# Kernel optimization log

Hardware: AMD Instinct MI355X
Metric: run time of the kernel (lower is better)

The kernel has to match this reference:

```python
import jax, jax.numpy as jnp
import numpy as np

G, K, N, T = 16, 2048, 2048, 16384  # groups, in_features, out_features, total_tokens


def setup_inputs() -> dict:
    key = jax.random.key(0)
    k1, k2 = jax.random.split(key)
    hidden_states = jax.random.normal(k1, (T, K), dtype=jnp.float32)
    # kaiming_uniform_(a=sqrt(5)) on [G, K, N] -> bound = sqrt(6 / ((1 + 5) * fan_in)) = 1/sqrt(K)
    bound = 1.0 / np.sqrt(K)
    weight = jax.random.uniform(k2, (G, K, N), dtype=jnp.float32, minval=-bound, maxval=bound)
    tokens_per_group = T // G
    tokens_per_expert = jnp.full((G,), tokens_per_group, dtype=jnp.int32)
    # offsets[0] = 0, offsets[i] = start of group i (matches _group_sizes_from_offsets)
    offsets = jnp.arange(G, dtype=jnp.int32) * tokens_per_group
    blockscale_offsets = offsets  # unused by the eager math path; carried for signature fidelity
    return {
        "hidden_states": hidden_states,
        "weight": weight,
        "offsets": offsets,
        "blockscale_offsets": blockscale_offsets,
        "tokens_per_expert": tokens_per_expert,
    }


def reference(hidden_states, weight, offsets, blockscale_offsets, tokens_per_expert):
    # Grouped (ragged) GEMM: rows [offsets[g] : offsets[g]+tokens_per_expert[g]] of
    # hidden_states are multiplied by weight[g] ([K, N]). tokens_per_expert equals the
    # group sizes derived from offsets in the torch module's eager fallback.
    # jax.lax.ragged_dot is the exact grouped-mm primitive (no dense [T,K,N] gather).
    return jax.lax.ragged_dot(hidden_states, weight, tokens_per_expert)
```

## Files before the change

### kernel.cpp

```cpp
#include <hip/hip_runtime.h>
#include <cstdint>
#include <cstddef>

#define GRP 16
#define KD  2048
#define ND  2048
#define TD  16384

#define BM 128
#define BN 128
#define BK 64
#define NT (KD / BK)

typedef __bf16 bf16x8 __attribute__((ext_vector_type(8)));
typedef float  f32x4  __attribute__((ext_vector_type(4)));

__device__ __forceinline__ uint32_t pk2bf(float x, float y) {
  uint32_t ux = __builtin_bit_cast(uint32_t, x);
  uint32_t uy = __builtin_bit_cast(uint32_t, y);
  ux += 0x7fffu + ((ux >> 16) & 1u);
  uy += 0x7fffu + ((uy >> 16) & 1u);
  return __builtin_amdgcn_perm(uy, ux, 0x07060302);
}

__device__ __forceinline__ int find_group(const int* tokens, int row0) {
  int g = GRP - 1, start = 0;
  for (int i = 0; i < GRP; ++i) {
    int sz = tokens[i];
    if (row0 < start + sz) { g = i; break; }
    start += sz;
  }
  return g;
}

__global__ __launch_bounds__(256, 2)
void fused_gemm(const float* __restrict__ A, const float* __restrict__ W,
                const int* __restrict__ tokens, float* __restrict__ C) {
  __shared__ uint16_t Alds[BM * BK];
  __shared__ uint16_t Blds[BN * BK];

  const int t    = threadIdx.x;
  const int n0   = blockIdx.x * BN;
  const int row0 = blockIdx.y * BM;

  const int g = find_group(tokens, row0);
  const float* Wg = W + (size_t)g * KD * ND;

  const int lane = t & 63;
  const int wid  = t >> 6;
  const int wm   = wid & 1;
  const int wn   = wid >> 1;
  const int l16  = lane & 15;
  const int quad = lane >> 4;

  const float* aptr[4];
  uint32_t*    adst[4];
  for (int i = 0; i < 4; ++i) {
    const int c  = t + 256 * i;
    const int r  = c >> 3;
    const int cl = c & 7;
    aptr[i] = A + (size_t)(row0 + r) * KD + cl * 8;
    adst[i] = (uint32_t*)&Alds[(r * 8 + (cl ^ (r & 7))) * 8];
  }

  const int nl = t & 127;
  const int bh = t >> 7;
  const float* bptr = Wg + (size_t)(bh * 32) * ND + n0 + nl;
  uint32_t* bdst[4];
  for (int c = 0; c < 4; ++c) {
    const int kc = bh * 4 + c;
    bdst[c] = (uint32_t*)&Blds[(nl * 8 + (kc ^ (nl & 7))) * 8];
  }

  int aoff[2][4], boff[2][4];
  for (int h = 0; h < 2; ++h) {
    for (int mi = 0; mi < 4; ++mi) {
      const int r = wm * 64 + mi * 16 + l16;
      aoff[h][mi] = r * BK + (((h * 4 + quad) ^ (r & 7)) * 8);
    }
    for (int ni = 0; ni < 4; ++ni) {
      const int r = wn * 64 + ni * 16 + l16;
      boff[h][ni] = r * BK + (((h * 4 + quad) ^ (r & 7)) * 8);
    }
  }

  f32x4 acc[4][4] = {};

  float4 ar[4][2];
  float  br[4][8];

  auto issue = [&](int k0) {
    #pragma unroll
    for (int i = 0; i < 4; ++i) {
      ar[i][0] = *(const float4*)(aptr[i] + k0);
      ar[i][1] = *(const float4*)(aptr[i] + k0 + 4);
    }
    const float* bp = bptr + (size_t)k0 * ND;
    #pragma unroll
    for (int c = 0; c < 4; ++c)
      #pragma unroll
      for (int j = 0; j < 8; ++j)
        br[c][j] = bp[(size_t)(c * 8 + j) * ND];
  };

  issue(0);

  for (int kt = 0; kt < NT; ++kt) {
    __syncthreads();

    #pragma unroll
    for (int i = 0; i < 4; ++i) {
      uint4 p;
      p.x = pk2bf(ar[i][0].x, ar[i][0].y);
      p.y = pk2bf(ar[i][0].z, ar[i][0].w);
      p.z = pk2bf(ar[i][1].x, ar[i][1].y);
      p.w = pk2bf(ar[i][1].z, ar[i][1].w);
      *(uint4*)adst[i] = p;
    }
    #pragma unroll
    for (int c = 0; c < 4; ++c) {
      uint4 p;
      p.x = pk2bf(br[c][0], br[c][1]);
      p.y = pk2bf(br[c][2], br[c][3]);
      p.z = pk2bf(br[c][4], br[c][5]);
      p.w = pk2bf(br[c][6], br[c][7]);
      *(uint4*)bdst[c] = p;
    }

    if (kt + 1 < NT) issue((kt + 1) * BK);

    __syncthreads();

    #pragma unroll
    for (int h = 0; h < 2; ++h) {
      bf16x8 af[4], bfr[4];
      #pragma unroll
      for (int mi = 0; mi < 4; ++mi) af[mi]  = *(const bf16x8*)&Alds[aoff[h][mi]];
      #pragma unroll
      for (int ni = 0; ni < 4; ++ni) bfr[ni] = *(const bf16x8*)&Blds[boff[h][ni]];
      #pragma unroll
      for (int mi = 0; mi < 4; ++mi)
        #pragma unroll
        for (int ni = 0; ni < 4; ++ni)
          acc[mi][ni] = __builtin_amdgcn_mfma_f32_16x16x32_bf16(af[mi], bfr[ni],
                                                                acc[mi][ni], 0, 0, 0);
    }
  }

  #pragma unroll
  for (int mi = 0; mi < 4; ++mi) {
    const int m = row0 + wm * 64 + mi * 16 + quad * 4;
    #pragma unroll
    for (int ni = 0; ni < 4; ++ni) {
      const int n = n0 + wn * 64 + ni * 16 + l16;
      #pragma unroll
      for (int r = 0; r < 4; ++r)
        C[(size_t)(m + r) * ND + n] = acc[mi][ni][r];
    }
  }
}

extern "C" void kernel_launch(void* const* d_in, const int* in_sizes, int n_in,
                              void* d_out, int out_size, void* d_ws, size_t ws_size,
                              hipStream_t stream) {
  const float* hidden = (const float*)d_in[0];
  const float* weight = (const float*)d_in[1];
  const int*   tokens = (const int*)d_in[4];
  float* out = (float*)d_out;
  (void)d_ws; (void)ws_size;

  fused_gemm<<<dim3(ND / BN, TD / BM), 256, 0, stream>>>(hidden, weight, tokens, out);
}
```

Measured before the change: 693.9 us.

## Double-buffer LDS tiles with one barrier per k-step and prefetch two ahead

Splits the A and B LDS tiles into two buffers. Each iteration converts and stores the next tile while MFMAs read the current one, and issues global loads two k-steps ahead, so one barrier per iteration replaces two. It also swaps the manual bf16 rounding for native casts and raises wave priority around the MFMA block. LDS use doubles to 64KB per block, which may limit occupancy at 2 blocks per CU, and the register lifetimes of the prefetched data grow.

```diff
diff --git a/kernel.cpp b/kernel.cpp
--- a/kernel.cpp
+++ b/kernel.cpp
@@ -15,14 +15,6 @@
 typedef __bf16 bf16x8 __attribute__((ext_vector_type(8)));
 typedef float  f32x4  __attribute__((ext_vector_type(4)));
 
-__device__ __forceinline__ uint32_t pk2bf(float x, float y) {
-  uint32_t ux = __builtin_bit_cast(uint32_t, x);
-  uint32_t uy = __builtin_bit_cast(uint32_t, y);
-  ux += 0x7fffu + ((ux >> 16) & 1u);
-  uy += 0x7fffu + ((uy >> 16) & 1u);
-  return __builtin_amdgcn_perm(uy, ux, 0x07060302);
-}
-
 __device__ __forceinline__ int find_group(const int* tokens, int row0) {
   int g = GRP - 1, start = 0;
   for (int i = 0; i < GRP; ++i) {
@@ -33,11 +25,24 @@
   return g;
 }
 
+__device__ __forceinline__ bf16x8 cvt8(float4 a, float4 b) {
+  bf16x8 v;
+  v[0] = (__bf16)a.x; v[1] = (__bf16)a.y; v[2] = (__bf16)a.z; v[3] = (__bf16)a.w;
+  v[4] = (__bf16)b.x; v[5] = (__bf16)b.y; v[6] = (__bf16)b.z; v[7] = (__bf16)b.w;
+  return v;
+}
+
+#define BAR() do {                                         \
+    asm volatile("s_waitcnt lgkmcnt(0)" ::: "memory");     \
+    __builtin_amdgcn_s_barrier();                          \
+    asm volatile("" ::: "memory");                         \
+  } while (0)
+
 __global__ __launch_bounds__(256, 2)
 void fused_gemm(const float* __restrict__ A, const float* __restrict__ W,
                 const int* __restrict__ tokens, float* __restrict__ C) {
-  __shared__ uint16_t Alds[BM * BK];
-  __shared__ uint16_t Blds[BN * BK];
+  __shared__ uint16_t Alds[2][BM * BK];
+  __shared__ uint16_t Blds[2][BN * BK];
 
   const int t    = threadIdx.x;
   const int n0   = blockIdx.x * BN;
@@ -54,30 +59,35 @@
   const int quad = lane >> 4;
 
   const float* aptr[4];
-  uint32_t*    adst[4];
+  int adst[4];
+  #pragma unroll
   for (int i = 0; i < 4; ++i) {
     const int c  = t + 256 * i;
     const int r  = c >> 3;
     const int cl = c & 7;
     aptr[i] = A + (size_t)(row0 + r) * KD + cl * 8;
-    adst[i] = (uint32_t*)&Alds[(r * 8 + (cl ^ (r & 7))) * 8];
+    adst[i] = (r * 8 + (cl ^ (r & 7))) * 8;
   }
 
   const int nl = t & 127;
   const int bh = t >> 7;
-  const float* bptr = Wg + (size_t)(bh * 32) * ND + n0 + nl;
-  uint32_t* bdst[4];
+  const float* bbase = Wg + (size_t)(bh * 32) * ND + n0 + nl;
+  int bdst[4];
+  #pragma unroll
   for (int c = 0; c < 4; ++c) {
     const int kc = bh * 4 + c;
-    bdst[c] = (uint32_t*)&Blds[(nl * 8 + (kc ^ (nl & 7))) * 8];
+    bdst[c] = (nl * 8 + (kc ^ (nl & 7))) * 8;
   }
 
   int aoff[2][4], boff[2][4];
+  #pragma unroll
   for (int h = 0; h < 2; ++h) {
+    #pragma unroll
     for (int mi = 0; mi < 4; ++mi) {
       const int r = wm * 64 + mi * 16 + l16;
       aoff[h][mi] = r * BK + (((h * 4 + quad) ^ (r & 7)) * 8);
     }
+    #pragma unroll
     for (int ni = 0; ni < 4; ++ni) {
       const int r = wn * 64 + ni * 16 + l16;
       boff[h][ni] = r * BK + (((h * 4 + quad) ^ (r & 7)) * 8);
@@ -95,49 +105,49 @@
       ar[i][0] = *(const float4*)(aptr[i] + k0);
       ar[i][1] = *(const float4*)(aptr[i] + k0 + 4);
     }
-    const float* bp = bptr + (size_t)k0 * ND;
     #pragma unroll
     for (int c = 0; c < 4; ++c)
       #pragma unroll
       for (int j = 0; j < 8; ++j)
-        br[c][j] = bp[(size_t)(c * 8 + j) * ND];
+        br[c][j] = bbase[(size_t)(k0 + c * 8 + j) * ND];
+  };
+
+  auto convert = [&](int buf) {
+    #pragma unroll
+    for (int i = 0; i < 4; ++i)
+      *(bf16x8*)&Alds[buf][adst[i]] = cvt8(ar[i][0], ar[i][1]);
+    #pragma unroll
+    for (int c = 0; c < 4; ++c) {
+      bf16x8 w;
+      #pragma unroll
+      for (int j = 0; j < 8; ++j) w[j] = (__bf16)br[c][j];
+      *(bf16x8*)&Blds[buf][bdst[c]] = w;
+    }
   };
 
   issue(0);
+  convert(0);
+  issue(BK);
+  BAR();
 
+  #pragma unroll 2
   for (int kt = 0; kt < NT; ++kt) {
-    __syncthreads();
+    const int cur = kt & 1;
+    const int nxt = cur ^ 1;
 
-    #pragma unroll
-    for (int i = 0; i < 4; ++i) {
-      uint4 p;
-      p.x = pk2bf(ar[i][0].x, ar[i][0].y);
-      p.y = pk2bf(ar[i][0].z, ar[i][0].w);
-      p.z = pk2bf(ar[i][1].x, ar[i][1].y);
-      p.w = pk2bf(ar[i][1].z, ar[i][1].w);
-      *(uint4*)adst[i] = p;
-    }
-    #pragma unroll
-    for (int c = 0; c < 4; ++c) {
-      uint4 p;
-      p.x = pk2bf(br[c][0], br[c][1]);
-      p.y = pk2bf(br[c][2], br[c][3]);
-      p.z = pk2bf(br[c][4], br[c][5]);
-      p.w = pk2bf(br[c][6], br[c][7]);
-      *(uint4*)bdst[c] = p;
+    if (kt + 1 < NT) {
+      convert(nxt);
+      if (kt + 2 < NT) issue((kt + 2) * BK);
     }
 
-    if (kt + 1 < NT) issue((kt + 1) * BK);
-
-    __syncthreads();
-
+    __builtin_amdgcn_s_setprio(1);
     #pragma unroll
     for (int h = 0; h < 2; ++h) {
       bf16x8 af[4], bfr[4];
       #pragma unroll
-      for (int mi = 0; mi < 4; ++mi) af[mi]  = *(const bf16x8*)&Alds[aoff[h][mi]];
+      for (int mi = 0; mi < 4; ++mi) af[mi]  = *(const bf16x8*)&Alds[cur][aoff[h][mi]];
       #pragma unroll
-      for (int ni = 0; ni < 4; ++ni) bfr[ni] = *(const bf16x8*)&Blds[boff[h][ni]];
+      for (int ni = 0; ni < 4; ++ni) bfr[ni] = *(const bf16x8*)&Blds[cur][boff[h][ni]];
       #pragma unroll
       for (int mi = 0; mi < 4; ++mi)
         #pragma unroll
@@ -145,6 +155,9 @@
           acc[mi][ni] = __builtin_amdgcn_mfma_f32_16x16x32_bf16(af[mi], bfr[ni],
                                                                 acc[mi][ni], 0, 0, 0);
     }
+    __builtin_amdgcn_s_setprio(0);
+
+    BAR();
   }
 
   #pragma unroll
```

Result: faster. 644.9 us (-7.1%).
